# Performance work log

Measured on AMD Instinct MI355X. Metric: run time of the kernel, lower is better.

## Reference

```python
import jax, jax.numpy as jnp
import numpy as np

H, D = 12, 64  # num_heads, head_dim (embed_size=768)


def setup_inputs() -> dict:
    key = jax.random.key(0)
    k1, k2, k3 = jax.random.split(key, 3)
    z = jax.random.normal(k1, (2, 2048, 768), dtype=jnp.float32)
    W = jax.random.normal(k2, (768, 3 * H * D), dtype=jnp.float32) * (768 ** -0.5)
    bias = jax.random.normal(k3, (3 * H * D,), dtype=jnp.float32) * 0.02
    return {"z": z, "W": W, "bias": bias}


def reference(z, W, bias):
    b, n, _ = z.shape
    # fused QKV projection, reshaped exactly as torch: (b, n, h, d, 3)
    kvq = (z @ W + bias).reshape(b, n, H, D, 3)
    k = kvq[..., 0]  # (b, n, h, d)
    v = kvq[..., 1]
    q = kvq[..., 2]
    qk = jnp.einsum("bqhd,bkhd->bhqk", q, k)  # full O(n^2) scores
    # NOTE: original module scales AFTER softmax (faithful reproduction of bug)
    a = jax.nn.softmax(qk, axis=-1) * (D ** -0.5)
    sa = jnp.einsum("bhqk,bkhd->bqhd", a, v)
    return sa.reshape(b, n, H * D)
```

## Files before the change

kernel.cpp:

```cpp
#include <hip/hip_runtime.h>
#include <hip/hip_bf16.h>
#include <math.h>

#define BB 2
#define NN 2048
#define HH 12
#define DD 64
#define EE 768
#define FF 2304

typedef __attribute__((ext_vector_type(8))) _Float16 f16x8;
typedef __attribute__((ext_vector_type(4))) short bf16x4;
typedef __attribute__((ext_vector_type(4))) float f32x4;
typedef __attribute__((address_space(3))) unsigned int lds_u32;
typedef const __attribute__((address_space(1))) unsigned int glb_u32;

static __device__ __forceinline__ ushort f2bf(float x) {
    __hip_bfloat16 h = __float2bfloat16(x);
    return *reinterpret_cast<ushort*>(&h);
}

__global__ __launch_bounds__(256) void convert_zw(
    const float* __restrict__ z, const float* __restrict__ W,
    _Float16* __restrict__ Zf, _Float16* __restrict__ Wtf)
{
    __shared__ float T[64][65];
    const int t = threadIdx.x;
    if (blockIdx.x < 1536) {
        const int i = (blockIdx.x * 256 + t) * 8;
        const float4 a = *(const float4*)&z[i];
        const float4 b = *(const float4*)&z[i + 4];
        const float v[8] = {a.x, a.y, a.z, a.w, b.x, b.y, b.z, b.w};
        f16x8 h8;
#pragma unroll
        for (int j = 0; j < 8; ++j) h8[j] = (_Float16)v[j];
        *(f16x8*)&Zf[i] = h8;
    } else {
        const int r  = blockIdx.x - 1536;
        const int c0 = (r % 36) * 64;
        const int k0 = (r / 36) * 64;
#pragma unroll
        for (int i = 0; i < 4; ++i) {
            const int row = i * 16 + (t >> 4);
            const int c4  = (t & 15) * 4;
            const float4 w4 = *(const float4*)&W[(size_t)(k0 + row) * FF + c0 + c4];
            T[row][c4 + 0] = w4.x; T[row][c4 + 1] = w4.y;
            T[row][c4 + 2] = w4.z; T[row][c4 + 3] = w4.w;
        }
        __syncthreads();
#pragma unroll
        for (int u = 0; u < 2; ++u) {
            const int id = t + u * 256;
            const int c  = id >> 3;
            const int kc = id & 7;
            f16x8 h8;
#pragma unroll
            for (int j = 0; j < 8; ++j) h8[j] = (_Float16)T[kc * 8 + j][c];
            *(f16x8*)&Wtf[(size_t)(c0 + c) * EE + k0 + kc * 8] = h8;
        }
    }
}

__global__ __launch_bounds__(256, 2) void qkv_gemm(
    const _Float16* __restrict__ Zf, const _Float16* __restrict__ Wtf,
    const float* __restrict__ bias,
    _Float16* __restrict__ Qf, _Float16* __restrict__ Kp,
    ushort* __restrict__ Vp)
{
    __shared__ __align__(16) _Float16 As[128 * 64];
    __shared__ __align__(16) _Float16 Bs[128 * 64];

    const int tid  = threadIdx.x;
    const int wave = tid >> 6;
    const int lane = tid & 63;
    const int l4   = lane & 15;
    const int quad = lane >> 4;
    const int wx   = wave & 1;
    const int wy   = wave >> 1;
    const int row0 = blockIdx.y * 128;
    const int col0 = blockIdx.x * 128;

    int offAB[4], ldsoff[4];
#pragma unroll
    for (int u = 0; u < 4; ++u) {
        const int g = tid + u * 256;
        offAB[u]  = (g >> 3) * EE + (g & 7) * 8;
        ldsoff[u] = (u * 256 + wave * 64) * 16;
    }
    const _Float16* ZB = Zf  + (size_t)row0 * EE;
    const _Float16* WB = Wtf + (size_t)col0 * EE;

    f32x4 acc[4][4];
#pragma unroll
    for (int mi = 0; mi < 4; ++mi)
#pragma unroll
        for (int ni = 0; ni < 4; ++ni) acc[mi][ni] = (f32x4){0.f, 0.f, 0.f, 0.f};

    for (int k0 = 0; k0 < EE; k0 += 64) {
#pragma unroll
        for (int u = 0; u < 4; ++u) {
            __builtin_amdgcn_global_load_lds((glb_u32*)(ZB + offAB[u] + k0),
                                             (lds_u32*)((char*)As + ldsoff[u]), 16, 0, 0);
            __builtin_amdgcn_global_load_lds((glb_u32*)(WB + offAB[u] + k0),
                                             (lds_u32*)((char*)Bs + ldsoff[u]), 16, 0, 0);
        }
        __syncthreads();

#pragma unroll
        for (int ks = 0; ks < 2; ++ks) {
            f16x8 aF[4], bF[4];
#pragma unroll
            for (int mi = 0; mi < 4; ++mi)
                aF[mi] = *(const f16x8*)&As[(wy * 64 + mi * 16 + l4) * 64 + ks * 32 + quad * 8];
#pragma unroll
            for (int ni = 0; ni < 4; ++ni)
                bF[ni] = *(const f16x8*)&Bs[(wx * 64 + ni * 16 + l4) * 64 + ks * 32 + quad * 8];
#pragma unroll
            for (int mi = 0; mi < 4; ++mi)
#pragma unroll
                for (int ni = 0; ni < 4; ++ni)
                    acc[mi][ni] = __builtin_amdgcn_mfma_f32_16x16x32_f16(
                        aF[mi], bF[ni], acc[mi][ni], 0, 0, 0);
        }
        __syncthreads();
    }

#pragma unroll
    for (int ni = 0; ni < 4; ++ni) {
        const int col = col0 + wx * 64 + ni * 16 + l4;
        const int h   = col / 192;
        const int rem = col - h * 192;
        const int d   = rem / 3;
        const int t3  = rem - d * 3;
        const float bv = bias[col];
#pragma unroll
        for (int mi = 0; mi < 4; ++mi) {
#pragma unroll
            for (int r = 0; r < 4; ++r) {
                const int grow = row0 + wy * 64 + mi * 16 + quad * 4 + r;
                const int bb = grow >> 11;
                const int q  = grow & 2047;
                const int bh = bb * HH + h;
                const float val = acc[mi][ni][r] + bv;
                const int s  = q >> 4;
                const int ko = q & 15;
                if (t3 == 0) {
                    const int dc = d >> 5, dd = d & 31;
                    Kp[(size_t)bh * 131072 + s * 1024 + dc * 512 +
                       ((dd >> 3) * 16 + ko) * 8 + (dd & 7)] = (_Float16)val;
                } else if (t3 == 1) {
                    const int dt = d >> 4, l4d = d & 15;
                    Vp[(size_t)bh * 131072 + s * 1024 + dt * 256 +
                       ((ko >> 2) * 16 + l4d) * 4 + (ko & 3)] = f2bf(val);
                } else {
                    Qf[((size_t)bh * NN + q) * DD + d] = (_Float16)(val * 1.44269504f);
                }
            }
        }
    }
}

__global__ __launch_bounds__(256, 3) void attn_kernel(
    const _Float16* __restrict__ Kp, const ushort* __restrict__ Vp,
    const _Float16* __restrict__ Qf, float* __restrict__ out)
{
    __shared__ __align__(16) float Red[3 * 16 * 64 * 4];
    __shared__ float lRed[3][4][16];

    const int tid  = threadIdx.x;
    const int wave = tid >> 6;
    const int lane = tid & 63;
    const int l4   = lane & 15;
    const int quad = lane >> 4;
    const int bh   = blockIdx.x;
    const int q0   = blockIdx.y * 64;

    const _Float16* QB = Qf + (size_t)bh * NN * DD;

    f16x8 qF[4][2];
#pragma unroll
    for (int qc = 0; qc < 4; ++qc) {
        const _Float16* qb = QB + (size_t)(q0 + qc * 16 + l4) * DD + quad * 8;
        qF[qc][0] = *(const f16x8*)qb;
        qF[qc][1] = *(const f16x8*)(qb + 32);
    }

    f32x4 O[4][4];
#pragma unroll
    for (int dt = 0; dt < 4; ++dt)
#pragma unroll
        for (int qc = 0; qc < 4; ++qc) O[dt][qc] = (f32x4){0.f, 0.f, 0.f, 0.f};
    f32x4 lC[4];
#pragma unroll
    for (int qc = 0; qc < 4; ++qc) lC[qc] = (f32x4){0.f, 0.f, 0.f, 0.f};
    const bf16x4 onesA = {(short)0x3F80, (short)0x3F80, (short)0x3F80, (short)0x3F80};

    const _Float16* kp = Kp + (size_t)bh * 131072 + wave * 1024 + lane * 8;
    const ushort*   vp = Vp + (size_t)bh * 131072 + wave * 1024 + lane * 4;

    f16x8 kc0 = *(const f16x8*)kp;
    f16x8 kc1 = *(const f16x8*)(kp + 512);
    bf16x4 vc[4];
#pragma unroll
    for (int dt = 0; dt < 4; ++dt)
        vc[dt] = *(const bf16x4*)(vp + dt * 256);

    for (int it = 0; it < 32; ++it) {
        f16x8 kn0, kn1;
        bf16x4 vn[4];
        if (it < 31) {
            const _Float16* kpn = kp + (it + 1) * 4096;
            const ushort*   vpn = vp + (it + 1) * 4096;
            kn0 = *(const f16x8*)kpn;
            kn1 = *(const f16x8*)(kpn + 512);
#pragma unroll
            for (int dt = 0; dt < 4; ++dt)
                vn[dt] = *(const bf16x4*)(vpn + dt * 256);
        }

        bf16x4 pF[4];
#pragma unroll
        for (int qc = 0; qc < 4; ++qc) {
            f32x4 s = {0.f, 0.f, 0.f, 0.f};
            s = __builtin_amdgcn_mfma_f32_16x16x32_f16(kc0, qF[qc][0], s, 0, 0, 0);
            s = __builtin_amdgcn_mfma_f32_16x16x32_f16(kc1, qF[qc][1], s, 0, 0, 0);
#pragma unroll
            for (int r = 0; r < 4; ++r)
                pF[qc][r] = (short)f2bf(__builtin_amdgcn_exp2f(s[r]));
        }

#pragma unroll
        for (int qc = 0; qc < 4; ++qc) {
#pragma unroll
            for (int dt = 0; dt < 4; ++dt)
                O[dt][qc] = __builtin_amdgcn_mfma_f32_16x16x16bf16_1k(
                    vc[dt], pF[qc], O[dt][qc], 0, 0, 0);
            lC[qc] = __builtin_amdgcn_mfma_f32_16x16x16bf16_1k(
                onesA, pF[qc], lC[qc], 0, 0, 0);
        }

        if (it < 31) {
            kc0 = kn0; kc1 = kn1;
#pragma unroll
            for (int dt = 0; dt < 4; ++dt) vc[dt] = vn[dt];
        }
    }

    f32x4* RedV = (f32x4*)Red;
    if (wave > 0) {
        const int wb = (wave - 1) * 16 * 64;
#pragma unroll
        for (int dt = 0; dt < 4; ++dt)
#pragma unroll
            for (int qc = 0; qc < 4; ++qc)
                RedV[wb + (dt * 4 + qc) * 64 + lane] = O[dt][qc];
        if (lane < 16) {
#pragma unroll
            for (int qc = 0; qc < 4; ++qc) lRed[wave - 1][qc][l4] = lC[qc][0];
        }
    }
    __syncthreads();
    if (wave == 0) {
        const int bb = bh / HH;
        const int h  = bh - bb * HH;
        float inv[4];
#pragma unroll
        for (int qc = 0; qc < 4; ++qc)
            inv[qc] = 0.125f /
                (lC[qc][0] + lRed[0][qc][l4] + lRed[1][qc][l4] + lRed[2][qc][l4]);
#pragma unroll
        for (int dt = 0; dt < 4; ++dt) {
#pragma unroll
            for (int qc = 0; qc < 4; ++qc) {
                f32x4 o = O[dt][qc];
#pragma unroll
                for (int w = 0; w < 3; ++w) {
                    const f32x4 o2 = RedV[w * 16 * 64 + (dt * 4 + qc) * 64 + lane];
                    o[0] += o2[0]; o[1] += o2[1]; o[2] += o2[2]; o[3] += o2[3];
                }
                const int q = q0 + qc * 16 + l4;
                float4 ov;
                ov.x = o[0] * inv[qc]; ov.y = o[1] * inv[qc];
                ov.z = o[2] * inv[qc]; ov.w = o[3] * inv[qc];
                *(float4*)&out[((size_t)(bb * NN + q)) * (HH * DD) + h * DD +
                               dt * 16 + quad * 4] = ov;
            }
        }
    }
}

extern "C" void kernel_launch(void* const* d_in, const int* in_sizes, int n_in,
                              void* d_out, int out_size, void* d_ws, size_t ws_size,
                              hipStream_t stream)
{
    const float* z    = (const float*)d_in[0];
    const float* W    = (const float*)d_in[1];
    const float* bias = (const float*)d_in[2];
    float* out = (float*)d_out;

    const size_t N1 = (size_t)BB * HH * NN * DD;
    const size_t NW = (size_t)EE * FF;
    _Float16* ws  = (_Float16*)d_ws;
    _Float16* Zf  = ws;
    _Float16* Wtf = ws + N1;
    _Float16* Qf  = ws + N1 + NW;
    _Float16* Kp  = ws + 2 * N1 + NW;
    ushort*   Vp  = (ushort*)(ws + 3 * N1 + NW);

    convert_zw<<<dim3(1968), 256, 0, stream>>>(z, W, Zf, Wtf);
    qkv_gemm<<<dim3(18, 32), 256, 0, stream>>>(Zf, Wtf, bias, Qf, Kp, Vp);
    attn_kernel<<<dim3(24, 32), 256, 0, stream>>>(Kp, Vp, Qf, out);
}
```

Before: 143.8 us.

## Software-pipeline QK scores one iteration ahead of exp and PV MFMAs

Restructures the attention inner loop so the QK^T MFMAs for the next key tile run in the same iteration as the exp2 and PV MFMAs of the current tile. K loads are prefetched two tiles ahead and V one tile ahead. The goal is to hide exp/convert latency and MFMA dependency stalls by interleaving independent work. In exchange it holds an extra score accumulator set in registers (16 more VGPRs), which could raise register pressure or reduce occupancy.

```diff
diff --git a/kernel.cpp b/kernel.cpp
--- a/kernel.cpp
+++ b/kernel.cpp
@@ -198,52 +198,74 @@
     const _Float16* kp = Kp + (size_t)bh * 131072 + wave * 1024 + lane * 8;
     const ushort*   vp = Vp + (size_t)bh * 131072 + wave * 1024 + lane * 4;
 
-    f16x8 kc0 = *(const f16x8*)kp;
-    f16x8 kc1 = *(const f16x8*)(kp + 512);
-    bf16x4 vc[4];
+    const f16x8 kA0 = *(const f16x8*)kp;
+    const f16x8 kA1 = *(const f16x8*)(kp + 512);
+    bf16x4 vF[4];
 #pragma unroll
     for (int dt = 0; dt < 4; ++dt)
-        vc[dt] = *(const bf16x4*)(vp + dt * 256);
+        vF[dt] = *(const bf16x4*)(vp + dt * 256);
+    f16x8 kB0 = *(const f16x8*)(kp + 4096);
+    f16x8 kB1 = *(const f16x8*)(kp + 4096 + 512);
+
+    f32x4 sS[4];
+#pragma unroll
+    for (int qc = 0; qc < 4; ++qc) {
+        f32x4 s = {0.f, 0.f, 0.f, 0.f};
+        s = __builtin_amdgcn_mfma_f32_16x16x32_f16(kA0, qF[qc][0], s, 0, 0, 0);
+        s = __builtin_amdgcn_mfma_f32_16x16x32_f16(kA1, qF[qc][1], s, 0, 0, 0);
+        sS[qc] = s;
+    }
 
     for (int it = 0; it < 32; ++it) {
-        f16x8 kn0, kn1;
-        bf16x4 vn[4];
+        f16x8 kN0, kN1;
+        bf16x4 vN[4];
+        if (it < 30) {
+            const _Float16* kpn = kp + (it + 2) * 4096;
+            kN0 = *(const f16x8*)kpn;
+            kN1 = *(const f16x8*)(kpn + 512);
+        }
         if (it < 31) {
-            const _Float16* kpn = kp + (it + 1) * 4096;
-            const ushort*   vpn = vp + (it + 1) * 4096;
-            kn0 = *(const f16x8*)kpn;
-            kn1 = *(const f16x8*)(kpn + 512);
+            const ushort* vpn = vp + (it + 1) * 4096;
 #pragma unroll
             for (int dt = 0; dt < 4; ++dt)
-                vn[dt] = *(const bf16x4*)(vpn + dt * 256);
+                vN[dt] = *(const bf16x4*)(vpn + dt * 256);
+        }
+
+        f32x4 sN[4];
+        if (it < 31) {
+#pragma unroll
+            for (int qc = 0; qc < 4; ++qc) {
+                f32x4 s = {0.f, 0.f, 0.f, 0.f};
+                s = __builtin_amdgcn_mfma_f32_16x16x32_f16(kB0, qF[qc][0], s, 0, 0, 0);
+                s = __builtin_amdgcn_mfma_f32_16x16x32_f16(kB1, qF[qc][1], s, 0, 0, 0);
+                sN[qc] = s;
+            }
         }
 
         bf16x4 pF[4];
 #pragma unroll
-        for (int qc = 0; qc < 4; ++qc) {
-            f32x4 s = {0.f, 0.f, 0.f, 0.f};
-            s = __builtin_amdgcn_mfma_f32_16x16x32_f16(kc0, qF[qc][0], s, 0, 0, 0);
-            s = __builtin_amdgcn_mfma_f32_16x16x32_f16(kc1, qF[qc][1], s, 0, 0, 0);
+        for (int qc = 0; qc < 4; ++qc)
 #pragma unroll
             for (int r = 0; r < 4; ++r)
-                pF[qc][r] = (short)f2bf(__builtin_amdgcn_exp2f(s[r]));
-        }
+                pF[qc][r] = (short)f2bf(__builtin_amdgcn_exp2f(sS[qc][r]));
 
 #pragma unroll
         for (int qc = 0; qc < 4; ++qc) {
 #pragma unroll
             for (int dt = 0; dt < 4; ++dt)
                 O[dt][qc] = __builtin_amdgcn_mfma_f32_16x16x16bf16_1k(
-                    vc[dt], pF[qc], O[dt][qc], 0, 0, 0);
+                    vF[dt], pF[qc], O[dt][qc], 0, 0, 0);
             lC[qc] = __builtin_amdgcn_mfma_f32_16x16x16bf16_1k(
                 onesA, pF[qc], lC[qc], 0, 0, 0);
         }
 
         if (it < 31) {
-            kc0 = kn0; kc1 = kn1;
-#pragma unroll
-            for (int dt = 0; dt < 4; ++dt) vc[dt] = vn[dt];
-        }
+#pragma unroll
+            for (int qc = 0; qc < 4; ++qc) sS[qc] = sN[qc];
+#pragma unroll
+            for (int dt = 0; dt < 4; ++dt) vF[dt] = vN[dt];
+        }
+        if (it < 30) { kB0 = kN0; kB1 = kN1; }
     }
 
     f32x4* RedV = (f32x4*)Red;
```

Measured after the change: 144.2 us. About the same (+0.2%).
